# Kernel tuning notes

Hardware: AMD Instinct MI355X
Metric: run time of the kernel (lower is better)

Reference implementation:

```python
import jax, jax.numpy as jnp
import numpy as np

TOP_K = 4
N_GROUP = 4
TOPK_GROUP = 2
ROUTED_SCALE = 2.5


def grouped_matmul(x, w, group_sizes):
    """x: [N, k] rows sorted by expert; w: [E, k, n]; group_sizes: [E] int32."""
    if hasattr(jax.lax, "ragged_dot"):
        return jax.lax.ragged_dot(x, w, group_sizes)
    # Fallback: expert id per row via searchsorted on cumulative counts, masked dense GEMMs.
    eid = jnp.searchsorted(jnp.cumsum(group_sizes), jnp.arange(x.shape[0]), side="right")
    out = jnp.zeros((x.shape[0], w.shape[-1]), x.dtype)
    for e in range(w.shape[0]):
        out = out + jnp.where((eid == e)[:, None], x @ w[e], 0.0)
    return out


def setup_inputs() -> dict:
    key = jax.random.key(0)
    ks = jax.random.split(key, 9)
    b, s, h, i, E = 2, 2048, 1024, 512, 32
    return {
        "hidden_states": jax.random.normal(ks[0], (b, s, h), jnp.float32),
        "gate_weight": jax.random.normal(ks[1], (E, h), jnp.float32) * 0.02,
        "expert_bias": jnp.zeros((E,), jnp.float32),
        "w_gate": jax.random.normal(ks[2], (E, h, i), jnp.float32) * 0.02,
        "w_up": jax.random.normal(ks[3], (E, h, i), jnp.float32) * 0.02,
        "w_down": jax.random.normal(ks[4], (E, i, h), jnp.float32) * 0.02,
        "ws_gate": jax.random.normal(ks[5], (h, i), jnp.float32) * 0.02,
        "ws_up": jax.random.normal(ks[6], (h, i), jnp.float32) * 0.02,
        "ws_down": jax.random.normal(ks[7], (i, h), jnp.float32) * 0.02,
    }


def reference(hidden_states, gate_weight, expert_bias, w_gate, w_up, w_down,
              ws_gate, ws_up, ws_down):
    b, s, h = hidden_states.shape
    E = gate_weight.shape[0]
    x = hidden_states.reshape(-1, h)          # [T, h]
    T = x.shape[0]

    # --- gate (LLaDA2MoeGate) ---
    logits = x.astype(jnp.float32) @ gate_weight.T.astype(jnp.float32)  # [T, E]
    scores = jax.nn.sigmoid(logits)
    s_rt = scores + expert_bias
    # group-limited top-k: score each group by sum of its top-2 experts
    grp = s_rt.reshape(T, N_GROUP, E // N_GROUP)
    grp_score = jax.lax.top_k(grp, 2)[0].sum(-1)                         # [T, G]
    _, gidx = jax.lax.top_k(grp_score, TOPK_GROUP)
    gmask = jnp.zeros((T, N_GROUP), jnp.float32).at[jnp.arange(T)[:, None], gidx].set(1.0)
    smask = jnp.repeat(gmask, E // N_GROUP, axis=1)                      # [T, E]
    masked = jnp.where(smask > 0, s_rt, -jnp.inf)
    _, topk_idx = jax.lax.top_k(masked, TOP_K)                           # [T, K]
    tw = jnp.take_along_axis(scores, topk_idx, axis=1)
    tw = tw / (tw.sum(-1, keepdims=True) + 1e-20) * ROUTED_SCALE         # [T, K]

    # --- moe_infer: sort by expert, grouped GEMMs, unsort + weighted combine ---
    flat = topk_idx.reshape(-1)                                          # [T*K]
    order = jnp.argsort(flat)
    xs = x[order // TOP_K]                                               # [N, h] sorted by expert
    counts = jnp.bincount(flat, length=E).astype(jnp.int32)
    g = grouped_matmul(xs, w_gate, counts)
    u = grouped_matmul(xs, w_up, counts)
    out_s = grouped_matmul(jax.nn.silu(g) * u, w_down, counts)           # [N, h]
    y = jnp.zeros_like(out_s).at[order].set(out_s)                       # unsort
    y = (y.reshape(T, TOP_K, h) * tw[:, :, None]).sum(1)

    # --- shared experts (SwiGLU MLP on identity) ---
    shared = (jax.nn.silu(x @ ws_gate) * (x @ ws_up)) @ ws_down
    y = (y + shared).reshape(b, s, h)
    return y, logits.reshape(b, s, E), topk_idx.reshape(b, s, TOP_K)
```

## Files before the change

### kernel.cpp

```cpp
#include <hip/hip_runtime.h>
#include <stdint.h>

typedef __attribute__((ext_vector_type(8))) short short8;
typedef __attribute__((ext_vector_type(4))) float f32x4;

#define NR_ROUTED 16384
#define NROWS     20480
#define MAXTILES  192

__device__ __forceinline__ float bf2f(unsigned short h) {
  return __uint_as_float(((unsigned)h) << 16);
}
__device__ __forceinline__ unsigned short f2bf(float f) {
  unsigned u = __float_as_uint(f);
  u = (u + 0x7FFFu + ((u >> 16) & 1u)) >> 16;
  return (unsigned short)u;
}

__global__ void cast_x_kernel(const float* __restrict__ x, unsigned short* __restrict__ xb) {
  int idx = blockIdx.x * 256 + threadIdx.x;
  float4 v = ((const float4*)x)[idx];
  ushort4 o;
  o.x = f2bf(v.x); o.y = f2bf(v.y); o.z = f2bf(v.z); o.w = f2bf(v.w);
  ((ushort4*)xb)[idx] = o;
}

__global__ void tcast_kernel(const float* __restrict__ src0, const float* __restrict__ src1,
                             unsigned short* __restrict__ dst, int Kd, int Nd, int n_off) {
  __shared__ float tl[64][65];
  int tilesK = Kd >> 6;
  int tk = blockIdx.x % tilesK, tn = blockIdx.x / tilesK;
  int e = blockIdx.y;
  const float* src = (e < 32) ? (src0 + (size_t)e * Kd * Nd) : src1;
  int k0 = tk * 64, n0 = tn * 64;
  int tid = threadIdx.x;
#pragma unroll
  for (int p = 0; p < 4; ++p) {
    int f = p * 256 + tid;
    int r = f >> 4, c4 = (f & 15) * 4;
    float4 v = *(const float4*)(src + (size_t)(k0 + r) * Nd + n0 + c4);
    tl[c4 + 0][r] = v.x; tl[c4 + 1][r] = v.y; tl[c4 + 2][r] = v.z; tl[c4 + 3][r] = v.w;
  }
  __syncthreads();
#pragma unroll
  for (int p = 0; p < 4; ++p) {
    int f = p * 256 + tid;
    int n = f >> 4, kc = (f & 15) * 4;
    ushort4 o;
    o.x = f2bf(tl[n][kc + 0]); o.y = f2bf(tl[n][kc + 1]);
    o.z = f2bf(tl[n][kc + 2]); o.w = f2bf(tl[n][kc + 3]);
    *(ushort4*)(dst + ((size_t)e * 1024 + n_off + n0 + n) * Kd + k0 + kc) = o;
  }
}

__global__ void routing_kernel(const float* __restrict__ x, const float* __restrict__ gw,
                               const float* __restrict__ bias,
                               float* __restrict__ logits_out, float* __restrict__ topk_f,
                               int* __restrict__ topk_i, float* __restrict__ tw,
                               int* __restrict__ counts) {
  __shared__ float xs[1024];
  __shared__ float lg[32];
  __shared__ float sc[32];
  __shared__ float srt[32];
  int t = blockIdx.x, tid = threadIdx.x;
  ((float4*)xs)[tid] = ((const float4*)(x + (size_t)t * 1024))[tid];
  __syncthreads();
  int e = tid >> 3, part = tid & 7;
  const float* gwe = gw + (size_t)e * 1024;
  float acc = 0.f;
#pragma unroll 8
  for (int j = 0; j < 32; ++j) {
    int c = part * 4 + j * 32;
    float4 xv = *(const float4*)(xs + c);
    float4 wv = *(const float4*)(gwe + c);
    acc += xv.x * wv.x + xv.y * wv.y + xv.z * wv.z + xv.w * wv.w;
  }
  acc += __shfl_xor(acc, 1);
  acc += __shfl_xor(acc, 2);
  acc += __shfl_xor(acc, 4);
  if (part == 0) { lg[e] = acc; logits_out[(size_t)t * 32 + e] = acc; }
  __syncthreads();
  if (tid < 32) {
    float sg = 1.f / (1.f + expf(-lg[tid]));
    sc[tid] = sg;
    srt[tid] = sg + bias[tid];
  }
  __syncthreads();
  if (tid == 0) {
    float gs[4];
#pragma unroll
    for (int g = 0; g < 4; ++g) {
      float m1 = -1e30f, m2 = -1e30f;
      for (int i2 = 0; i2 < 8; ++i2) {
        float v = srt[g * 8 + i2];
        if (v > m1) { m2 = m1; m1 = v; }
        else if (v > m2) { m2 = v; }
      }
      gs[g] = m1 + m2;
    }
    int g1 = 0;
    for (int g = 1; g < 4; ++g) if (gs[g] > gs[g1]) g1 = g;
    int g2 = -1;
    for (int g = 0; g < 4; ++g) {
      if (g == g1) continue;
      if (g2 < 0 || gs[g] > gs[g2]) g2 = g;
    }
    unsigned allowed = (0xFFu << (g1 * 8)) | (0xFFu << (g2 * 8));
    int idxs[4];
    float wsum = 1e-20f;
    for (int k = 0; k < 4; ++k) {
      int best = 0; float bv = -1e30f; int found = -1;
      for (int e2 = 0; e2 < 32; ++e2) {
        if (!((allowed >> e2) & 1u)) continue;
        float v = srt[e2];
        if (v > bv) { bv = v; found = e2; }
      }
      best = found;
      allowed &= ~(1u << best);
      idxs[k] = best;
      wsum += sc[best];
    }
    float scale = 2.5f / wsum;
    for (int k = 0; k < 4; ++k) {
      int ii = idxs[k];
      topk_i[t * 4 + k] = ii;
      topk_f[t * 4 + k] = (float)ii;
      tw[t * 4 + k] = sc[ii] * scale;
      atomicAdd(&counts[ii], 1);
    }
  }
}

__global__ void build_tiles_kernel(const int* __restrict__ counts, int* __restrict__ cursor,
                                   int4* __restrict__ table, int* __restrict__ n_tiles) {
  if (threadIdx.x != 0) return;
  int base = 0, nt = 0;
  for (int e = 0; e < 32; ++e) {
    cursor[e] = base;
    int n = counts[e];
    for (int j = 0; j < n; j += 128) {
      int rem = n - j;
      table[nt] = make_int4(e, base + j, rem < 128 ? rem : 128, 0);
      ++nt;
    }
    base += n;
  }
  for (int j = 0; j < 32; ++j) {
    table[nt] = make_int4(32, NR_ROUTED + j * 128, 128, 0);
    ++nt;
  }
  *n_tiles = nt;
}

__global__ void assign_kernel(const int* __restrict__ topk_i, int* __restrict__ cursor,
                              int* __restrict__ perm, int* __restrict__ pos) {
  int idx = blockIdx.x * 256 + threadIdx.x;
  if (idx < NR_ROUTED) {
    int e = topk_i[idx];
    int p = atomicAdd(&cursor[e], 1);
    perm[p] = idx >> 2;
    pos[idx] = p;
  } else {
    perm[idx] = idx - NR_ROUTED;
  }
}

__global__ __launch_bounds__(256, 2) void gemm_kernel(
    const unsigned short* __restrict__ A, const unsigned short* __restrict__ B,
    unsigned short* __restrict__ C, const int* __restrict__ perm,
    const int4* __restrict__ table, const int* __restrict__ n_tiles,
    int K, int use_perm) {
  __shared__ unsigned short Al[128 * 64];
  __shared__ unsigned short Bl[128 * 64];
  if ((int)blockIdx.x >= *n_tiles) return;
  int4 te = table[blockIdx.x];
  int eidx = te.x, row_start = te.y, nrows = te.z;
  int n0 = blockIdx.y * 128;
  int tid = threadIdx.x, lane = tid & 63, wave = tid >> 6;
  int wr = wave >> 1, wc = wave & 1;

  const unsigned short* aBase[4];
  const unsigned short* bBase[4];
  unsigned short* aL[4];
  unsigned short* bL[4];
#pragma unroll
  for (int i = 0; i < 4; ++i) {
    int s = wave * 64 + i * 256 + lane;
    int row = s >> 3, cseg = s & 7;
    int rowg = row_start + row;
    int tok = use_perm ? perm[rowg] : rowg;
    aBase[i] = A + (size_t)tok * K + cseg * 8;
    bBase[i] = B + (size_t)eidx * 1024 * K + (size_t)(n0 + row) * K + cseg * 8;
    aL[i] = &Al[(wave * 64 + i * 256) * 8];
    bL[i] = &Bl[(wave * 64 + i * 256) * 8];
  }
  f32x4 acc[4][4];
  f32x4 z = {0.f, 0.f, 0.f, 0.f};
#pragma unroll
  for (int a = 0; a < 4; ++a)
#pragma unroll
    for (int b = 0; b < 4; ++b) acc[a][b] = z;

  for (int k0 = 0; k0 < K; k0 += 64) {
#pragma unroll
    for (int i = 0; i < 4; ++i) {
      __builtin_amdgcn_global_load_lds(
          (const __attribute__((address_space(1))) unsigned int*)(aBase[i] + k0),
          (__attribute__((address_space(3))) unsigned int*)aL[i], 16, 0, 0);
      __builtin_amdgcn_global_load_lds(
          (const __attribute__((address_space(1))) unsigned int*)(bBase[i] + k0),
          (__attribute__((address_space(3))) unsigned int*)bL[i], 16, 0, 0);
    }
    asm volatile("s_waitcnt vmcnt(0)" ::: "memory");
    __syncthreads();
#pragma unroll
    for (int ks = 0; ks < 2; ++ks) {
      short8 af[4], bfr[4];
#pragma unroll
      for (int rf = 0; rf < 4; ++rf) {
        int m = wr * 64 + rf * 16 + (lane & 15);
        af[rf] = *(const short8*)&Al[m * 64 + ks * 32 + (lane >> 4) * 8];
      }
#pragma unroll
      for (int cf = 0; cf < 4; ++cf) {
        int n = wc * 64 + cf * 16 + (lane & 15);
        bfr[cf] = *(const short8*)&Bl[n * 64 + ks * 32 + (lane >> 4) * 8];
      }
#pragma unroll
      for (int rf = 0; rf < 4; ++rf)
#pragma unroll
        for (int cf = 0; cf < 4; ++cf)
          acc[rf][cf] = __builtin_amdgcn_mfma_f32_16x16x32_bf16(af[rf], bfr[cf], acc[rf][cf], 0, 0, 0);
    }
    __syncthreads();
  }
  int q = lane >> 4, cl = lane & 15;
#pragma unroll
  for (int rf = 0; rf < 4; ++rf) {
#pragma unroll
    for (int r = 0; r < 4; ++r) {
      int rowl = wr * 64 + rf * 16 + q * 4 + r;
      if (rowl < nrows) {
        size_t rowg = (size_t)(row_start + rowl);
#pragma unroll
        for (int cf = 0; cf < 4; ++cf) {
          int colg = n0 + wc * 64 + cf * 16 + cl;
          C[rowg * 1024 + colg] = f2bf(acc[rf][cf][r]);
        }
      }
    }
  }
}

__global__ void silu_kernel(const unsigned short* __restrict__ gu, unsigned short* __restrict__ act) {
  int idx = blockIdx.x * 256 + threadIdx.x;
  int row = idx >> 7;
  int c = (idx & 127) * 4;
  ushort4 g4 = *(const ushort4*)(gu + (size_t)row * 1024 + c);
  ushort4 u4 = *(const ushort4*)(gu + (size_t)row * 1024 + 512 + c);
  ushort4 o;
  float g, u;
  g = bf2f(g4.x); u = bf2f(u4.x); o.x = f2bf(g / (1.f + expf(-g)) * u);
  g = bf2f(g4.y); u = bf2f(u4.y); o.y = f2bf(g / (1.f + expf(-g)) * u);
  g = bf2f(g4.z); u = bf2f(u4.z); o.z = f2bf(g / (1.f + expf(-g)) * u);
  g = bf2f(g4.w); u = bf2f(u4.w); o.w = f2bf(g / (1.f + expf(-g)) * u);
  *(ushort4*)(act + (size_t)row * 512 + c) = o;
}

__global__ void combine_kernel(const unsigned short* __restrict__ outs,
                               const int* __restrict__ pos, const float* __restrict__ tw,
                               float* __restrict__ y) {
  int t = blockIdx.x, tid = threadIdx.x;
  int c = tid * 4;
  ushort4 sv = *(const ushort4*)(outs + (size_t)(NR_ROUTED + t) * 1024 + c);
  float y0 = bf2f(sv.x), y1 = bf2f(sv.y), y2 = bf2f(sv.z), y3 = bf2f(sv.w);
#pragma unroll
  for (int k = 0; k < 4; ++k) {
    int p = pos[t * 4 + k];
    float w = tw[t * 4 + k];
    ushort4 v = *(const ushort4*)(outs + (size_t)p * 1024 + c);
    y0 += w * bf2f(v.x); y1 += w * bf2f(v.y); y2 += w * bf2f(v.z); y3 += w * bf2f(v.w);
  }
  float4 o = {y0, y1, y2, y3};
  *(float4*)(y + (size_t)t * 1024 + c) = o;
}

extern "C" void kernel_launch(void* const* d_in, const int* in_sizes, int n_in,
                              void* d_out, int out_size, void* d_ws, size_t ws_size,
                              hipStream_t stream) {
  const float* x       = (const float*)d_in[0];
  const float* gw      = (const float*)d_in[1];
  const float* bias    = (const float*)d_in[2];
  const float* w_gate  = (const float*)d_in[3];
  const float* w_up    = (const float*)d_in[4];
  const float* w_down  = (const float*)d_in[5];
  const float* ws_gate = (const float*)d_in[6];
  const float* ws_up   = (const float*)d_in[7];
  const float* ws_down = (const float*)d_in[8];

  char* ws = (char*)d_ws;
  size_t off = 0;
  auto alloc = [&](size_t bytes) {
    void* p = ws + off;
    off = (off + bytes + 255) & ~(size_t)255;
    return p;
  };
  unsigned short* wgu = (unsigned short*)alloc(33ull * 1024 * 1024 * 2);
  unsigned short* wd  = (unsigned short*)alloc(33ull * 1024 * 512 * 2);
  unsigned short* xb  = (unsigned short*)alloc(4096ull * 1024 * 2);
  unsigned short* gu  = (unsigned short*)alloc((size_t)NROWS * 1024 * 2);
  unsigned short* act = (unsigned short*)alloc((size_t)NROWS * 512 * 2);
  int*   counts = (int*)alloc(32 * 4);
  int*   cursor = (int*)alloc(32 * 4);
  int*   ntiles = (int*)alloc(256);
  int4*  table  = (int4*)alloc(256 * 16);
  int*   perm   = (int*)alloc(NROWS * 4);
  int*   topk_i = (int*)alloc(NR_ROUTED * 4);
  int*   pos    = (int*)alloc(NR_ROUTED * 4);
  float* tw     = (float*)alloc(NR_ROUTED * 4);
  (void)ws_size; (void)in_sizes; (void)n_in; (void)out_size;

  float* out_y      = (float*)d_out;
  float* out_logits = out_y + 4096ull * 1024;
  float* out_topk   = out_logits + 4096ull * 32;

  hipMemsetAsync(counts, 0, 32 * 4, stream);
  cast_x_kernel<<<4096, 256, 0, stream>>>(x, xb);
  tcast_kernel<<<dim3(128, 33), 256, 0, stream>>>(w_gate, ws_gate, wgu, 1024, 512, 0);
  tcast_kernel<<<dim3(128, 33), 256, 0, stream>>>(w_up,   ws_up,   wgu, 1024, 512, 512);
  tcast_kernel<<<dim3(128, 33), 256, 0, stream>>>(w_down, ws_down, wd,  512, 1024, 0);
  routing_kernel<<<4096, 256, 0, stream>>>(x, gw, bias, out_logits, out_topk, topk_i, tw, counts);
  build_tiles_kernel<<<1, 64, 0, stream>>>(counts, cursor, table, ntiles);
  assign_kernel<<<80, 256, 0, stream>>>(topk_i, cursor, perm, pos);
  gemm_kernel<<<dim3(MAXTILES, 8), 256, 0, stream>>>(xb, wgu, gu, perm, table, ntiles, 1024, 1);
  silu_kernel<<<10240, 256, 0, stream>>>(gu, act);
  gemm_kernel<<<dim3(MAXTILES, 8), 256, 0, stream>>>(act, wd, gu, perm, table, ntiles, 512, 0);
  combine_kernel<<<4096, 256, 0, stream>>>(gu, pos, tw, out_y);
}
```

Measured before the change: 528.6 us.

## Fuse bf16 cast of x into routing kernel and parallelize top-k with warp shuffles

The separate cast_x kernel is removed and the bf16 conversion of x is done inside the routing kernel, which already loads x rows into shared memory. Each block now handles 8 tokens, with each 64-lane wavefront handling two tokens (one lane per expert). Group scoring and top-k selection move from a single serial thread to warp-shuffle reductions on packed score/index keys. This saves one kernel launch and one full read of x, and removes the serialized routing logic. The cost is 32KB of shared memory per block and fewer blocks (512), which may reduce occupancy.

```diff
diff --git a/kernel.cpp b/kernel.cpp
--- a/kernel.cpp
+++ b/kernel.cpp
@@ -15,14 +15,6 @@
   unsigned u = __float_as_uint(f);
   u = (u + 0x7FFFu + ((u >> 16) & 1u)) >> 16;
   return (unsigned short)u;
-}
-
-__global__ void cast_x_kernel(const float* __restrict__ x, unsigned short* __restrict__ xb) {
-  int idx = blockIdx.x * 256 + threadIdx.x;
-  float4 v = ((const float4*)x)[idx];
-  ushort4 o;
-  o.x = f2bf(v.x); o.y = f2bf(v.y); o.z = f2bf(v.z); o.w = f2bf(v.w);
-  ((ushort4*)xb)[idx] = o;
 }
 
 __global__ void tcast_kernel(const float* __restrict__ src0, const float* __restrict__ src1,
@@ -53,81 +45,95 @@
   }
 }
 
-__global__ void routing_kernel(const float* __restrict__ x, const float* __restrict__ gw,
-                               const float* __restrict__ bias,
-                               float* __restrict__ logits_out, float* __restrict__ topk_f,
-                               int* __restrict__ topk_i, float* __restrict__ tw,
-                               int* __restrict__ counts) {
-  __shared__ float xs[1024];
-  __shared__ float lg[32];
-  __shared__ float sc[32];
-  __shared__ float srt[32];
-  int t = blockIdx.x, tid = threadIdx.x;
-  ((float4*)xs)[tid] = ((const float4*)(x + (size_t)t * 1024))[tid];
+__global__ __launch_bounds__(256) void routing_kernel(
+    const float* __restrict__ x, const float* __restrict__ gw,
+    const float* __restrict__ bias, unsigned short* __restrict__ xb,
+    float* __restrict__ logits_out, float* __restrict__ topk_f,
+    int* __restrict__ topk_i, float* __restrict__ tw,
+    int* __restrict__ counts) {
+  __shared__ float xs[8 * 1024];
+  int tid = threadIdx.x;
+  int tbase = blockIdx.x * 8;
+  const float4* xsrc = (const float4*)(x + (size_t)tbase * 1024);
+  float4* xd = (float4*)xs;
+#pragma unroll
+  for (int p = 0; p < 8; ++p) xd[p * 256 + tid] = xsrc[p * 256 + tid];
   __syncthreads();
-  int e = tid >> 3, part = tid & 7;
+  ushort4* xbd = (ushort4*)(xb + (size_t)tbase * 1024);
+#pragma unroll
+  for (int p = 0; p < 8; ++p) {
+    int g = p * 256 + tid;
+    float4 v = xd[g];
+    ushort4 o;
+    o.x = f2bf(v.x); o.y = f2bf(v.y); o.z = f2bf(v.z); o.w = f2bf(v.w);
+    xbd[g] = o;
+  }
+  int lane = tid & 63, w = tid >> 6;
+  int tok2 = lane >> 5, e = lane & 31, h = lane & 32;
+  int t = tbase + w * 2 + tok2;
+  const float* xrow = xs + (size_t)(w * 2 + tok2) * 1024;
   const float* gwe = gw + (size_t)e * 1024;
   float acc = 0.f;
 #pragma unroll 8
-  for (int j = 0; j < 32; ++j) {
-    int c = part * 4 + j * 32;
-    float4 xv = *(const float4*)(xs + c);
-    float4 wv = *(const float4*)(gwe + c);
+  for (int j = 0; j < 256; ++j) {
+    float4 xv = *(const float4*)(xrow + j * 4);
+    float4 wv = *(const float4*)(gwe + j * 4);
     acc += xv.x * wv.x + xv.y * wv.y + xv.z * wv.z + xv.w * wv.w;
   }
-  acc += __shfl_xor(acc, 1);
-  acc += __shfl_xor(acc, 2);
-  acc += __shfl_xor(acc, 4);
-  if (part == 0) { lg[e] = acc; logits_out[(size_t)t * 32 + e] = acc; }
-  __syncthreads();
-  if (tid < 32) {
-    float sg = 1.f / (1.f + expf(-lg[tid]));
-    sc[tid] = sg;
-    srt[tid] = sg + bias[tid];
-  }
-  __syncthreads();
-  if (tid == 0) {
-    float gs[4];
-#pragma unroll
-    for (int g = 0; g < 4; ++g) {
-      float m1 = -1e30f, m2 = -1e30f;
-      for (int i2 = 0; i2 < 8; ++i2) {
-        float v = srt[g * 8 + i2];
-        if (v > m1) { m2 = m1; m1 = v; }
-        else if (v > m2) { m2 = v; }
-      }
-      gs[g] = m1 + m2;
-    }
-    int g1 = 0;
-    for (int g = 1; g < 4; ++g) if (gs[g] > gs[g1]) g1 = g;
-    int g2 = -1;
-    for (int g = 0; g < 4; ++g) {
-      if (g == g1) continue;
-      if (g2 < 0 || gs[g] > gs[g2]) g2 = g;
-    }
-    unsigned allowed = (0xFFu << (g1 * 8)) | (0xFFu << (g2 * 8));
-    int idxs[4];
-    float wsum = 1e-20f;
-    for (int k = 0; k < 4; ++k) {
-      int best = 0; float bv = -1e30f; int found = -1;
-      for (int e2 = 0; e2 < 32; ++e2) {
-        if (!((allowed >> e2) & 1u)) continue;
-        float v = srt[e2];
-        if (v > bv) { bv = v; found = e2; }
-      }
-      best = found;
-      allowed &= ~(1u << best);
-      idxs[k] = best;
-      wsum += sc[best];
-    }
-    float scale = 2.5f / wsum;
-    for (int k = 0; k < 4; ++k) {
-      int ii = idxs[k];
-      topk_i[t * 4 + k] = ii;
-      topk_f[t * 4 + k] = (float)ii;
-      tw[t * 4 + k] = sc[ii] * scale;
-      atomicAdd(&counts[ii], 1);
-    }
+  logits_out[(size_t)t * 32 + e] = acc;
+  float sg = 1.f / (1.f + expf(-acc));
+  float srt = sg + bias[e];
+  float m1 = srt, m2 = -1e30f;
+#pragma unroll
+  for (int off = 1; off < 8; off <<= 1) {
+    float o1 = __shfl_xor(m1, off);
+    float o2 = __shfl_xor(m2, off);
+    if (o1 > m1) { m2 = fmaxf(m1, o2); m1 = o1; }
+    else         { m2 = fmaxf(m2, o1); }
+  }
+  float gsv = m1 + m2;
+  float q0 = __shfl(gsv, h + 0), q1 = __shfl(gsv, h + 8);
+  float q2 = __shfl(gsv, h + 16), q3 = __shfl(gsv, h + 24);
+  int ga = 0; float bv = q0;
+  if (q1 > bv) { ga = 1; bv = q1; }
+  if (q2 > bv) { ga = 2; bv = q2; }
+  if (q3 > bv) { ga = 3; bv = q3; }
+  int gb = -1; float bw = -1e30f;
+  if (ga != 0) { gb = 0; bw = q0; }
+  if (ga != 1 && q1 > bw) { gb = 1; bw = q1; }
+  if (ga != 2 && q2 > bw) { gb = 2; bw = q2; }
+  if (ga != 3 && q3 > bw) { gb = 3; bw = q3; }
+  unsigned allowed = (0xFFu << (ga * 8)) | (0xFFu << (gb * 8));
+  unsigned u = __float_as_uint(srt);
+  u = (u & 0x80000000u) ? ~u : (u | 0x80000000u);
+  unsigned long long key = ((unsigned long long)u << 32) | (unsigned)(31 - e);
+  if (!((allowed >> e) & 1u)) key = 0ull;
+  unsigned packed = 0;
+  float wsum = 0.f;
+#pragma unroll
+  for (int k = 0; k < 4; ++k) {
+    unsigned long long kk = key;
+#pragma unroll
+    for (int off = 1; off < 32; off <<= 1) {
+      unsigned long long o = __shfl_xor(kk, off);
+      if (o > kk) kk = o;
+    }
+    int ek = 31 - (int)(kk & 0xFFFFFFFFull);
+    float sge = __shfl(sg, h + ek);
+    wsum += sge;
+    packed |= (unsigned)ek << (8 * k);
+    if (e == ek) key = 0ull;
+  }
+  float scale = 2.5f / (wsum + 1e-20f);
+  int kq = e & 3;
+  int myek = (int)((packed >> (8 * kq)) & 0xFFu);
+  float mysg = __shfl(sg, h + myek);
+  if (e < 4) {
+    int t4 = t * 4 + e;
+    topk_i[t4] = myek;
+    topk_f[t4] = (float)myek;
+    tw[t4] = mysg * scale;
+    atomicAdd(&counts[myek], 1);
   }
 }
 
@@ -325,11 +331,10 @@
   float* out_topk   = out_logits + 4096ull * 32;
 
   hipMemsetAsync(counts, 0, 32 * 4, stream);
-  cast_x_kernel<<<4096, 256, 0, stream>>>(x, xb);
   tcast_kernel<<<dim3(128, 33), 256, 0, stream>>>(w_gate, ws_gate, wgu, 1024, 512, 0);
   tcast_kernel<<<dim3(128, 33), 256, 0, stream>>>(w_up,   ws_up,   wgu, 1024, 512, 512);
   tcast_kernel<<<dim3(128, 33), 256, 0, stream>>>(w_down, ws_down, wd,  512, 1024, 0);
-  routing_kernel<<<4096, 256, 0, stream>>>(x, gw, bias, out_logits, out_topk, topk_i, tw, counts);
+  routing_kernel<<<512, 256, 0, stream>>>(x, gw, bias, xb, out_logits, out_topk, topk_i, tw, counts);
   build_tiles_kernel<<<1, 64, 0, stream>>>(counts, cursor, table, ntiles);
   assign_kernel<<<80, 256, 0, stream>>>(topk_i, cursor, perm, pos);
   gemm_kernel<<<dim3(MAXTILES, 8), 256, 0, stream>>>(xb, wgu, gu, perm, table, ntiles, 1024, 1);
```

Result: faster. 503.8 us (-4.7%).
